# Performance work log

Hardware: AMD Instinct MI355X
Metric: run time of the kernel (lower is better)

The kernel has to match this reference:

```python
import jax, jax.numpy as jnp
import numpy as np

B, S, E, R = 128, 16, 512, 1000
_SCALE = np.float32(1.0 / np.sqrt(E))


def setup_inputs() -> dict:
    key = jax.random.key(0)
    ks = jax.random.split(key, 12)
    s = 1.0 / np.sqrt(E)
    u = lambda k, shape: jax.random.uniform(k, shape, jnp.float32, -s, s)
    emb = jax.random.normal(ks[0], (R + 1, E), jnp.float32).at[R].set(0.0)  # padding_idx row = 0
    return {
        "tokens": jax.random.randint(ks[11], (B, S), 0, R),
        "emb": emb,
        "W_ih": u(ks[1], (3 * E, E)), "W_hh": u(ks[2], (3 * E, E)),
        "b_ih": u(ks[3], (3 * E,)), "b_hh": u(ks[4], (3 * E,)),
        "w_fc": u(ks[5], (E,)), "b_fc": u(ks[6], ()),
        "Wq": u(ks[7], (E, E)), "bq": u(ks[8], (E,)),
        "Wk": u(ks[9], (E, E)), "bk": u(ks[10], (E,)),
    }


def _gru_step(x, h, W_ih, W_hh, b_ih, b_hh):
    # torch GRU cell: gates stacked as [r; z; n]
    gi = x @ W_ih.T + b_ih
    gh = h @ W_hh.T + b_hh
    ir, iz, inn = jnp.split(gi, 3, axis=-1)
    hr, hz, hn = jnp.split(gh, 3, axis=-1)
    r = jax.nn.sigmoid(ir + hr)
    z = jax.nn.sigmoid(iz + hz)
    n = jnp.tanh(inn + r * hn)
    return (1.0 - z) * n + z * h


def _attention(x, emb, Wq, bq, Wk, bk):
    # x: [B,1,E]; key = fc_k(cat(relation_emb, x)); scores = q k^T / sqrt(E)
    Bn = x.shape[0]
    rel = jnp.broadcast_to(emb[:R][None], (Bn, R, E))
    all_emb = jnp.concatenate([rel, x], axis=1)        # [B,R+1,E]
    q = x @ Wq.T + bq
    k = all_emb @ Wk.T + bk
    scores = jnp.einsum('bqe,bke->bqk', q, k) * _SCALE  # [B,1,R+1]
    return scores, all_emb


def _entropy(scores):
    lp = jax.nn.log_softmax(scores, axis=-1)
    return -jnp.sum(jnp.exp(lp) * lp, axis=-1)          # [B,1]


def _reduce(x, emb, W_ih, W_hh, b_ih, b_hh, w_fc, b_fc, Wq, bq, Wk, bk):
    Bn, L, Ed = x.shape
    if L > 2:
        # vectorized 2-step GRU over all adjacent pairs (replaces python while loop)
        h1 = _gru_step(x[:, :-1], jnp.zeros_like(x[:, :-1]), W_ih, W_hh, b_ih, b_hh)
        pairs = _gru_step(x[:, 1:], h1, W_ih, W_hh, b_ih, b_hh)   # [B,L-1,E]
        score = jax.nn.sigmoid(pairs @ w_fc + b_fc)               # [B,L-1]
        sel = jnp.argmax(score, axis=-1)                          # [B]
        barange = jnp.arange(Bn)
        pair = pairs[barange, sel][:, None]                       # [B,1,E]
        scores, all_emb = _attention(pair, emb, Wq, bq, Wk, bk)
        loss = _entropy(scores)
        prob = jax.nn.softmax(scores, axis=-1)                    # weightedAverage mask is all-False for seq_len=1
        merged = jnp.einsum('bqk,bke->bqe', prob, all_emb)[:, 0]  # [B,E]
        # output = inputs.detach().clone(); overwrite sel with merged; delete row sel+1
        out = jax.lax.stop_gradient(x).at[barange, sel].set(merged)
        j = jnp.arange(L - 1)[None]
        src = j + (j >= (sel + 1)[:, None])                       # skip zeroed row sel+1
        out = out[barange[:, None], src]                          # [B,L-1,E]
        return out, loss
    else:
        h1 = _gru_step(x[:, 0], jnp.zeros_like(x[:, 0]), W_ih, W_hh, b_ih, b_hh)
        h2 = _gru_step(x[:, 1], h1, W_ih, W_hh, b_ih, b_hh)
        return h2[:, None], jnp.zeros((Bn, 1), x.dtype)


def reference(tokens, emb, W_ih, W_hh, b_ih, b_hh, w_fc, b_fc, Wq, bq, Wk, bk):
    x = emb[tokens]                                               # [B,S,E]
    losses = []
    for _ in range(tokens.shape[1] - 1):
        x, l = _reduce(x, emb, W_ih, W_hh, b_ih, b_hh, w_fc, b_fc, Wq, bq, Wk, bk)
        losses.append(l)
    scores, _ = _attention(x, emb, Wq, bq, Wk, bk)                # x is [B,1,E]
    losses.append(_entropy(scores))
    return scores[:, 0], jnp.concatenate(losses, axis=-1)         # ([B,R+1], [B,S])
```

## Files before the change

### kernel.cpp

```cpp
#include <hip/hip_runtime.h>

#define B 128
#define S 16
#define E 512
#define R 1000
#define K3 1536
#define NW0 1920
#define NWS 256
#define NS (B * (R + 1))
#define SCALE 0.04419417382415922f

static __device__ __forceinline__ float sigm(float x) { return 1.f / (1.f + expf(-x)); }

static __device__ __forceinline__ float brsum(float v, float* sb) {
  int tid = threadIdx.x;
  sb[tid] = v; __syncthreads();
  for (int s = 128; s > 0; s >>= 1) {
    if (tid < s) sb[tid] += sb[tid + s];
    __syncthreads();
  }
  float r = sb[0]; __syncthreads();
  return r;
}
static __device__ __forceinline__ float brmax(float v, float* sb) {
  int tid = threadIdx.x;
  sb[tid] = v; __syncthreads();
  for (int s = 128; s > 0; s >>= 1) {
    if (tid < s) sb[tid] = fmaxf(sb[tid], sb[tid + s]);
    __syncthreads();
  }
  float r = sb[0]; __syncthreads();
  return r;
}
static __device__ __forceinline__ void brsum2(float v1, float v2, float* sb, float* sb2,
                                              float* o1, float* o2) {
  int tid = threadIdx.x;
  sb[tid] = v1; sb2[tid] = v2; __syncthreads();
  for (int s = 128; s > 0; s >>= 1) {
    if (tid < s) { sb[tid] += sb[tid + s]; sb2[tid] += sb2[tid + s]; }
    __syncthreads();
  }
  *o1 = sb[0]; *o2 = sb2[0]; __syncthreads();
}

#define TILE_FMA \
  _Pragma("unroll") \
  for (int k = 0; k < 16; ++k) { \
    float4 a4 = *(const float4*)&As[k][ty * 4]; \
    float4 w4 = *(const float4*)&Ws[k][tx * 4]; \
    acc[0][0] = fmaf(a4.x, w4.x, acc[0][0]); acc[0][1] = fmaf(a4.x, w4.y, acc[0][1]); \
    acc[0][2] = fmaf(a4.x, w4.z, acc[0][2]); acc[0][3] = fmaf(a4.x, w4.w, acc[0][3]); \
    acc[1][0] = fmaf(a4.y, w4.x, acc[1][0]); acc[1][1] = fmaf(a4.y, w4.y, acc[1][1]); \
    acc[1][2] = fmaf(a4.y, w4.z, acc[1][2]); acc[1][3] = fmaf(a4.y, w4.w, acc[1][3]); \
    acc[2][0] = fmaf(a4.z, w4.x, acc[2][0]); acc[2][1] = fmaf(a4.z, w4.y, acc[2][1]); \
    acc[2][2] = fmaf(a4.z, w4.z, acc[2][2]); acc[2][3] = fmaf(a4.z, w4.w, acc[2][3]); \
    acc[3][0] = fmaf(a4.w, w4.x, acc[3][0]); acc[3][1] = fmaf(a4.w, w4.y, acc[3][1]); \
    acc[3][2] = fmaf(a4.w, w4.z, acc[3][2]); acc[3][3] = fmaf(a4.w, w4.w, acc[3][3]); \
  }

#define TILE_FMA32 \
  _Pragma("unroll") \
  for (int k = 0; k < 16; ++k) { \
    float2 a2 = *(const float2*)&As[k][ty * 2]; \
    float4 w4 = *(const float4*)&Ws[k][tx * 4]; \
    acc[0][0] = fmaf(a2.x, w4.x, acc[0][0]); acc[0][1] = fmaf(a2.x, w4.y, acc[0][1]); \
    acc[0][2] = fmaf(a2.x, w4.z, acc[0][2]); acc[0][3] = fmaf(a2.x, w4.w, acc[0][3]); \
    acc[1][0] = fmaf(a2.y, w4.x, acc[1][0]); acc[1][1] = fmaf(a2.y, w4.y, acc[1][1]); \
    acc[1][2] = fmaf(a2.y, w4.z, acc[1][2]); acc[1][3] = fmaf(a2.y, w4.w, acc[1][3]); \
  }

__global__ __launch_bounds__(256) void k_gemm(const float* __restrict__ A, int lda, int M,
                                              const float* __restrict__ W, int N, int K,
                                              const float* __restrict__ bias, float scale,
                                              float* __restrict__ C, int ldc) {
  __shared__ float As[16][64];
  __shared__ float Ws[16][64];
  int tid = threadIdx.x;
  int mBase = blockIdx.y * 64;
  int nBase = blockIdx.x * 64;
  int tx = tid & 15, ty = tid >> 4;
  int li = tid & 63;
  int lk = (tid >> 6) * 4;
  float acc[4][4] = {{0.f,0.f,0.f,0.f},{0.f,0.f,0.f,0.f},{0.f,0.f,0.f,0.f},{0.f,0.f,0.f,0.f}};
  int m = mBase + li;
  const float* Arow = (m < M) ? (A + (size_t)m * lda) : nullptr;
  int n = nBase + li;
  const float* Wrow = (n < N) ? (W + (size_t)n * K) : nullptr;

  float4 av = Arow ? *(const float4*)(Arow + lk) : make_float4(0.f, 0.f, 0.f, 0.f);
  float4 wv = Wrow ? *(const float4*)(Wrow + lk) : make_float4(0.f, 0.f, 0.f, 0.f);

  for (int k0 = 0; k0 < K; k0 += 16) {
    As[lk + 0][li] = av.x; As[lk + 1][li] = av.y;
    As[lk + 2][li] = av.z; As[lk + 3][li] = av.w;
    Ws[lk + 0][li] = wv.x; Ws[lk + 1][li] = wv.y;
    Ws[lk + 2][li] = wv.z; Ws[lk + 3][li] = wv.w;
    __syncthreads();
    if (k0 + 16 < K) {
      av = Arow ? *(const float4*)(Arow + k0 + 16 + lk) : make_float4(0.f, 0.f, 0.f, 0.f);
      wv = Wrow ? *(const float4*)(Wrow + k0 + 16 + lk) : make_float4(0.f, 0.f, 0.f, 0.f);
    }
    TILE_FMA
    __syncthreads();
  }
#pragma unroll
  for (int r = 0; r < 4; ++r) {
    int mm = mBase + ty * 4 + r;
    if (mm >= M) continue;
#pragma unroll
    for (int c = 0; c < 4; ++c) {
      int nn = nBase + tx * 4 + c;
      if (nn >= N) continue;
      float v = acc[r][c] * scale;
      if (bias) v += bias[nn];
      C[(size_t)mm * ldc + nn] = v;
    }
  }
}

__global__ __launch_bounds__(256) void k_gemmD(const float* __restrict__ A, int lda, int M,
                                               const float* __restrict__ W1, int N1,
                                               const float* __restrict__ b1,
                                               float* __restrict__ C1, int ldc1,
                                               const float* __restrict__ W2, int N2,
                                               float* __restrict__ C2, int ldc2, int K) {
  __shared__ float As[16][64];
  __shared__ float Ws[16][64];
  int tid = threadIdx.x;
  int mBase = blockIdx.y * 64;
  int nBase = blockIdx.x * 64;
  int tx = tid & 15, ty = tid >> 4;
  int li = tid & 63;
  int lk = (tid >> 6) * 4;
  float acc[4][4] = {{0.f,0.f,0.f,0.f},{0.f,0.f,0.f,0.f},{0.f,0.f,0.f,0.f},{0.f,0.f,0.f,0.f}};
  int m = mBase + li;
  const float* Arow = (m < M) ? (A + (size_t)m * lda) : nullptr;
  int n = nBase + li;
  const float* Wrow = nullptr;
  if (n < N1) Wrow = W1 + (size_t)n * K;
  else if (n < N1 + N2) Wrow = W2 + (size_t)(n - N1) * K;

  float4 av = Arow ? *(const float4*)(Arow + lk) : make_float4(0.f, 0.f, 0.f, 0.f);
  float4 wv = Wrow ? *(const float4*)(Wrow + lk) : make_float4(0.f, 0.f, 0.f, 0.f);

  for (int k0 = 0; k0 < K; k0 += 16) {
    As[lk + 0][li] = av.x; As[lk + 1][li] = av.y;
    As[lk + 2][li] = av.z; As[lk + 3][li] = av.w;
    Ws[lk + 0][li] = wv.x; Ws[lk + 1][li] = wv.y;
    Ws[lk + 2][li] = wv.z; Ws[lk + 3][li] = wv.w;
    __syncthreads();
    if (k0 + 16 < K) {
      av = Arow ? *(const float4*)(Arow + k0 + 16 + lk) : make_float4(0.f, 0.f, 0.f, 0.f);
      wv = Wrow ? *(const float4*)(Wrow + k0 + 16 + lk) : make_float4(0.f, 0.f, 0.f, 0.f);
    }
    TILE_FMA
    __syncthreads();
  }
#pragma unroll
  for (int r = 0; r < 4; ++r) {
    int mm = mBase + ty * 4 + r;
    if (mm >= M) continue;
#pragma unroll
    for (int c = 0; c < 4; ++c) {
      int nn = nBase + tx * 4 + c;
      if (nn < N1) {
        float v = acc[r][c];
        if (b1) v += b1[nn];
        C1[(size_t)mm * ldc1 + nn] = v;
      } else if (nn < N1 + N2) {
        C2[(size_t)mm * ldc2 + (nn - N1)] = acc[r][c];
      }
    }
  }
}

static __device__ void dev_tr64(float (*t)[65], int tid, const float* __restrict__ src,
                                int Cc, float* __restrict__ dst, int ldd, int bx, int by) {
  int tx = tid & 15, ty = tid >> 4;
  int rb = by * 64, cb = bx * 64;
#pragma unroll
  for (int i = 0; i < 4; ++i) {
    int r = rb + ty + i * 16;
    float4 v = *(const float4*)(src + (size_t)r * Cc + cb + tx * 4);
    t[ty + i * 16][tx * 4 + 0] = v.x; t[ty + i * 16][tx * 4 + 1] = v.y;
    t[ty + i * 16][tx * 4 + 2] = v.z; t[ty + i * 16][tx * 4 + 3] = v.w;
  }
  __syncthreads();
#pragma unroll
  for (int i = 0; i < 4; ++i) {
    int c = cb + ty + i * 16;
    float4 v;
    v.x = t[tx * 4 + 0][ty + i * 16]; v.y = t[tx * 4 + 1][ty + i * 16];
    v.z = t[tx * 4 + 2][ty + i * 16]; v.w = t[tx * 4 + 3][ty + i * 16];
    *(float4*)(dst + (size_t)c * ldd + rb + tx * 4) = v;
  }
}

__global__ __launch_bounds__(256) void k_prep(const float* __restrict__ Wq,
                                              const float* __restrict__ Wk,
                                              const float* __restrict__ Wih,
                                              float* __restrict__ Wbig,
                                              int* __restrict__ pos,
                                              int* __restrict__ wlb,
                                              int* __restrict__ wlL,
                                              int* __restrict__ wlR,
                                              float* __restrict__ outp,
                                              float* __restrict__ Gbig,
                                              const float* __restrict__ bq,
                                              const float* __restrict__ bk,
                                              float* __restrict__ v12,
                                              float* __restrict__ bw,
                                              float* __restrict__ wv3,
                                              float* __restrict__ c0s) {
  __shared__ float t[64][65];
  int blk = blockIdx.x, tid = threadIdx.x;
  if (blk < 192) {
    dev_tr64(t, tid, Wih, E, Wbig + (size_t)1024 * K3, K3, blk & 7, blk >> 3);
  } else if (blk < 200) {
    int idx = (blk - 192) * 256 + tid;
    if (idx < B * 16) pos[idx] = idx & 15;
    if (idx < NW0) {
      wlb[idx] = idx / 15;
      int i = idx % 15;
      wlL[idx] = i;
      wlR[idx] = i + 1;
    }
    if (idx < B) outp[NS + idx * 16 + 14] = 0.f;
  } else if (blk < 208) {
    int idx = (blk - 200) * 256 + tid;
    for (int i = idx; i < 24 * K3; i += 8 * 256) Wbig[(size_t)1000 * K3 + i] = 0.f;
  } else if (blk < 272) {
    int j = blk - 208;
    int fT = (j & 7) * 64, iT = (j >> 3) * 64;
    float (*As)[64] = (float(*)[64])&t[0][0];
    float (*Ws)[64] = (float(*)[64])&t[20][0];
    int tx = tid & 15, ty = tid >> 4;
    int li = tid & 63, lk = (tid >> 6) * 4;
    float acc[4][4] = {{0.f,0.f,0.f,0.f},{0.f,0.f,0.f,0.f},{0.f,0.f,0.f,0.f},{0.f,0.f,0.f,0.f}};
    float a0 = Wq[(size_t)(lk + 0) * E + iT + li];
    float a1 = Wq[(size_t)(lk + 1) * E + iT + li];
    float a2 = Wq[(size_t)(lk + 2) * E + iT + li];
    float a3 = Wq[(size_t)(lk + 3) * E + iT + li];
    float w0 = Wk[(size_t)(lk + 0) * E + fT + li];
    float w1 = Wk[(size_t)(lk + 1) * E + fT + li];
    float w2 = Wk[(size_t)(lk + 2) * E + fT + li];
    float w3 = Wk[(size_t)(lk + 3) * E + fT + li];
    for (int e0 = 0; e0 < E; e0 += 16) {
      As[lk + 0][li] = a0; As[lk + 1][li] = a1;
      As[lk + 2][li] = a2; As[lk + 3][li] = a3;
      Ws[lk + 0][li] = w0; Ws[lk + 1][li] = w1;
      Ws[lk + 2][li] = w2; Ws[lk + 3][li] = w3;
      __syncthreads();
      if (e0 + 16 < E) {
        a0 = Wq[(size_t)(e0 + 16 + lk + 0) * E + iT + li];
        a1 = Wq[(size_t)(e0 + 16 + lk + 1) * E + iT + li];
        a2 = Wq[(size_t)(e0 + 16 + lk + 2) * E + iT + li];
        a3 = Wq[(size_t)(e0 + 16 + lk + 3) * E + iT + li];
        w0 = Wk[(size_t)(e0 + 16 + lk + 0) * E + fT + li];
        w1 = Wk[(size_t)(e0 + 16 + lk + 1) * E + fT + li];
        w2 = Wk[(size_t)(e0 + 16 + lk + 2) * E + fT + li];
        w3 = Wk[(size_t)(e0 + 16 + lk + 3) * E + fT + li];
      }
      TILE_FMA
      __syncthreads();
    }
#pragma unroll
    for (int r = 0; r < 4; ++r)
#pragma unroll
      for (int c = 0; c < 4; ++c)
        Gbig[(size_t)(1000 + iT + ty * 4 + r) * E + fT + tx * 4 + c] = acc[r][c];
  } else if (blk < 274) {
    int i = (blk - 272) * 256 + tid;
    float s = 0.f;
    for (int e = 0; e < E; ++e) s += Wq[(size_t)e * E + i] * bk[e] + bq[e] * Wk[(size_t)e * E + i];
    v12[i] = s;
  } else if (blk < 276) {
    int i = (blk - 274) * 256 + tid;
    float s = 0.f;
    for (int e = 0; e < E; ++e) s += bk[e] * Wq[(size_t)e * E + i];
    bw[i] = s;
  } else if (blk < 278) {
    int f = (blk - 276) * 256 + tid;
    float s = 0.f;
    for (int e = 0; e < E; ++e) s += bq[e] * Wk[(size_t)e * E + f];
    wv3[f] = s;
  } else {
    float* sb = &t[0][0];
    float p = 0.f;
    for (int e = tid; e < E; e += 256) p += bq[e] * bk[e];
    float s = brsum(p, sb);
    if (tid == 0) c0s[0] = s;
  }
}

__global__ __launch_bounds__(256) void k_setupB(const int* __restrict__ tokens,
                                                const float* __restrict__ Wbig,
                                                const float* __restrict__ bih,
                                                const float* __restrict__ bhh,
                                                const float* __restrict__ emb,
                                                const float* __restrict__ wv3,
                                                float* __restrict__ GI,
                                                float* __restrict__ H1V,
                                                float* __restrict__ SCT,
                                                float* __restrict__ gb) {
  int blk = blockIdx.x, tid = threadIdx.x;
  if (blk < 1000) {
    const float* ew = Wbig + (size_t)blk * K3;
    float* h = H1V + (size_t)blk * E;
    for (int e = tid; e < E; e += 256) {
      float g0 = ew[e] + bih[e];
      float g1 = ew[E + e] + bih[E + e];
      float g2 = ew[2 * E + e] + bih[2 * E + e];
      float r = sigm(g0 + bhh[e]);
      float z = sigm(g1 + bhh[E + e]);
      h[e] = (1.f - z) * tanhf(g2 + r * bhh[2 * E + e]);
    }
  } else if (blk < 1000 + B * S) {
    int p = blk - 1000;
    int tok = tokens[p];
    const float4* src = (const float4*)(Wbig + (size_t)tok * K3);
    const float4* bv = (const float4*)bih;
    float4* dst = (float4*)(GI + (size_t)p * K3);
    for (int i = tid; i < K3 / 4; i += 256) {
      float4 a = src[i], b = bv[i];
      dst[i] = make_float4(a.x + b.x, a.y + b.y, a.z + b.z, a.w + b.w);
    }
  } else if (blk < 1000 + B * S + 8) {
    int rb = blk - (1000 + B * S);
    for (int m = rb * 16; m < rb * 16 + 16; ++m) {
      float* r = SCT + (size_t)m * K3;
      for (int n = tid; n < 1512; n += 256) r[n] = 0.f;
    }
  } else {
    int r = (blk - (1000 + B * S + 8)) * 256 + tid;
    if (r < R) {
      const float* er = emb + (size_t)r * E;
      float s = 0.f;
      for (int f = 0; f < E; ++f) s += er[f] * wv3[f];
      gb[r] = s;
    }
  }
}

__global__ __launch_bounds__(256) void k_pairc0(const int* __restrict__ tokens,
                                                const float* __restrict__ GI,
                                                const float* __restrict__ GHCV,
                                                const float* __restrict__ H1V,
                                                const float* __restrict__ wfc,
                                                const float* __restrict__ bfc,
                                                float* __restrict__ PAIR,
                                                float* __restrict__ SCR,
                                                float* __restrict__ H1P,
                                                float* __restrict__ GHCP) {
  __shared__ float sb[256];
  int w = blockIdx.x, tid = threadIdx.x;
  int b = w / 15, i = w % 15;
  int lp = b * 16 + i;
  int tok = tokens[lp];
  const float* gr = GI + (size_t)(lp + 1) * K3;
  const float* gh = GHCV + (size_t)tok * K3;
  const float* h = H1V + (size_t)tok * E;
  float* ghp = GHCP + (size_t)lp * K3;
  float* hp = H1P + (size_t)lp * E;
  float* p = PAIR + (size_t)lp * E;
  float part = 0.f;
  for (int e = tid; e < E; e += 256) {
    float g0 = gh[e], g1 = gh[E + e], g2 = gh[2 * E + e], he = h[e];
    ghp[e] = g0; ghp[E + e] = g1; ghp[2 * E + e] = g2; hp[e] = he;
    float r = sigm(gr[e] + g0);
    float z = sigm(gr[E + e] + g1);
    float n = tanhf(gr[2 * E + e] + r * g2);
    float pv = (1.f - z) * n + z * he;
    p[e] = pv;
    part += pv * wfc[e];
  }
  float d = brsum(part, sb);
  if (tid == 0) SCR[lp] = sigm(d + bfc[0]);
}

__global__ __launch_bounds__(256) void k_h1c(const int* __restrict__ xdst,
                                             const float* __restrict__ GI,
                                             const float* __restrict__ bhh,
                                             float* __restrict__ H1P) {
  int p = xdst[blockIdx.x], tid = threadIdx.x;
  const float* gi = GI + (size_t)p * K3;
  float* h = H1P + (size_t)p * E;
  for (int e = tid; e < E; e += 256) {
    float r = sigm(gi[e] + bhh[e]);
    float z = sigm(gi[E + e] + bhh[E + e]);
    h[e] = (1.f - z) * tanhf(gi[2 * E + e] + r * bhh[2 * E + e]);
  }
}

__global__ __launch_bounds__(256) void k_ghcs(const int* __restrict__ xdst,
                                              const float* __restrict__ H1P,
                                              const float* __restrict__ Whh,
                                              float* __restrict__ GHCP) {
  __shared__ float As[16][32];
  __shared__ float Ws[16][64];
  __shared__ int sp[32];
  int tid = threadIdx.x;
  int nBase = blockIdx.x * 64;
  int mBase = blockIdx.y * 32;
  int kbeg = blockIdx.z * 256;
  if (tid < 32) sp[tid] = xdst[mBase + tid];
  __syncthreads();
  int tx = tid & 15, ty = tid >> 4;
  int ar = tid & 31, ak = (tid >> 5) * 2;
  int li = tid & 63, lk = (tid >> 6) * 4;
  float acc[2][4] = {{0.f,0.f,0.f,0.f},{0.f,0.f,0.f,0.f}};
  const float* Arow = H1P + (size_t)sp[ar] * E + kbeg;
  const float* Wrow = Whh + (size_t)(nBase + li) * E + kbeg;
  float2 av = *(const float2*)(Arow + ak);
  float4 wv = *(const float4*)(Wrow + lk);
  for (int k0 = 0; k0 < 256; k0 += 16) {
    As[ak + 0][ar] = av.x; As[ak + 1][ar] = av.y;
    Ws[lk + 0][li] = wv.x; Ws[lk + 1][li] = wv.y;
    Ws[lk + 2][li] = wv.z; Ws[lk + 3][li] = wv.w;
    __syncthreads();
    if (k0 + 16 < 256) {
      av = *(const float2*)(Arow + k0 + 16 + ak);
      wv = *(const float4*)(Wrow + k0 + 16 + lk);
    }
    TILE_FMA32
    __syncthreads();
  }
#pragma unroll
  for (int r = 0; r < 2; ++r) {
    size_t crow = (size_t)sp[ty * 2 + r] * K3;
#pragma unroll
    for (int c = 0; c < 4; ++c) {
      int nn = nBase + tx * 4 + c;
      atomicAdd(&GHCP[crow + nn], acc[r][c]);
    }
  }
}

__global__ __launch_bounds__(256) void k_pairc(const int* __restrict__ wlb,
                                               const int* __restrict__ wlL,
                                               const int* __restrict__ wlR,
                                               const float* __restrict__ GI,
                                               const float* __restrict__ GHCP,
                                               const float* __restrict__ H1P,
                                               const float* __restrict__ wfc,
                                               const float* __restrict__ bfc,
                                               float* __restrict__ PAIR,
                                               float* __restrict__ SCR) {
  __shared__ float sb[256];
  int w = blockIdx.x, tid = threadIdx.x;
  int b = wlb[w], ls = wlL[w], rs = wlR[w];
  int lp = b * 16 + ls;
  const float* gr = GI + (size_t)(b * 16 + rs) * K3;
  const float* gh = GHCP + (size_t)lp * K3;
  const float* h = H1P + (size_t)lp * E;
  float* p = PAIR + (size_t)lp * E;
  float part = 0.f;
  for (int e = tid; e < E; e += 256) {
    float r = sigm(gr[e] + gh[e]);
    float z = sigm(gr[E + e] + gh[E + e]);
    float n = tanhf(gr[2 * E + e] + r * gh[2 * E + e]);
    float pv = (1.f - z) * n + z * h[e];
    p[e] = pv;
    part += pv * wfc[e];
  }
  float d = brsum(part, sb);
  if (tid == 0) SCR[b * 16 + ls] = sigm(d + bfc[0]);
}

__global__ __launch_bounds__(256) void k_qscsel(const float* __restrict__ PAIR,
                                                const float* __restrict__ SCR,
                                                const int* __restrict__ pin,
                                                int* __restrict__ pout,
                                                int* __restrict__ wlb,
                                                int* __restrict__ wlL,
                                                int* __restrict__ wlR,
                                                int* __restrict__ xdst,
                                                const float* __restrict__ Gbig,
                                                float* __restrict__ SCT,
                                                float* __restrict__ GI,
                                                const float* __restrict__ bih,
                                                float* __restrict__ GHCP,
                                                const float* __restrict__ bhh,
                                                int P, int finalMode) {
  __shared__ float As[16][32];
  __shared__ float Ws[16][64];
  __shared__ int sxd[32];
  int tid = threadIdx.x;
  int nBase = blockIdx.x * 64;
  int mBase = blockIdx.y * 32;
  int kbeg = blockIdx.z * 256;
  if (tid < 32) {
    int b = mBase + tid;
    if (finalMode) {
      int xr = b * 16 + pin[b * 16];
      sxd[tid] = xr;
      if (blockIdx.x == 0 && blockIdx.z == 0) xdst[b] = xr;
    } else {
      int L = P + 1;
      int lp[16];
      for (int i = 0; i < L; ++i) lp[i] = pin[b * 16 + i];
      float best = -1e30f; int sel = 0;
      for (int i = 0; i < P; ++i) {
        float v = SCR[b * 16 + lp[i]];
        if (v > best) { best = v; sel = i; }
      }
      int r1i = (sel + 2 < L) ? sel + 2 : L - 1;
      int l1 = lp[sel], r1 = lp[r1i];
      int l0 = (sel > 0) ? lp[sel - 1] : l1;
      int r0 = (sel > 0) ? lp[sel] : r1;
      sxd[tid] = b * 16 + l1;
      if (blockIdx.x == 0 && blockIdx.z == 0) {
        wlb[2 * b] = b;     wlL[2 * b] = l0;     wlR[2 * b] = r0;
        wlb[2 * b + 1] = b; wlL[2 * b + 1] = l1; wlR[2 * b + 1] = r1;
        xdst[b] = b * 16 + l1;
        for (int i = 0; i < L - 1; ++i)
          pout[b * 16 + i] = (i <= sel) ? lp[i] : lp[i + 1];
      }
    }
  }
  __syncthreads();
  if (!finalMode && blockIdx.z == 1) {
    if (blockIdx.x < 16) {
#pragma unroll
      for (int r = 0; r < 2; ++r) {
        float* g = GI + (size_t)sxd[blockIdx.x * 2 + r] * K3;
        for (int i = tid; i < K3; i += 256) g[i] = bih[i];
      }
    } else {
#pragma unroll
      for (int r = 0; r < 4; ++r) {
        float* g = GHCP + (size_t)sxd[(blockIdx.x - 16) * 4 + r] * K3;
        for (int i = tid; i < K3; i += 256) g[i] = bhh[i];
      }
    }
  }
  int tx = tid & 15, ty = tid >> 4;
  int ar = tid & 31, ak = (tid >> 5) * 2;
  int li = tid & 63, lk = (tid >> 6) * 4;
  float acc[2][4] = {{0.f,0.f,0.f,0.f},{0.f,0.f,0.f,0.f}};
  const float* Arow = PAIR + (size_t)sxd[ar] * E + kbeg;
  int n = nBase + li;
  const float* Wrow = (n < 1512) ? (Gbig + (size_t)n * E + kbeg) : nullptr;
  float2 av = *(const float2*)(Arow + ak);
  float4 wv = Wrow ? *(const float4*)(Wrow + lk) : make_float4(0.f, 0.f, 0.f, 0.f);
  for (int k0 = 0; k0 < 256; k0 += 16) {
    As[ak + 0][ar] = av.x; As[ak + 1][ar] = av.y;
    Ws[lk + 0][li] = wv.x; Ws[lk + 1][li] = wv.y;
    Ws[lk + 2][li] = wv.z; Ws[lk + 3][li] = wv.w;
    __syncthreads();
    if (k0 + 16 < 256) {
      av = *(const float2*)(Arow + k0 + 16 + ak);
      wv = Wrow ? *(const float4*)(Wrow + k0 + 16 + lk) : make_float4(0.f, 0.f, 0.f, 0.f);
    }
    TILE_FMA32
    __syncthreads();
  }
#pragma unroll
  for (int r = 0; r < 2; ++r) {
    int mm = mBase + ty * 2 + r;
#pragma unroll
    for (int c = 0; c < 4; ++c) {
      int nn = nBase + tx * 4 + c;
      if (nn < 1512) atomicAdd(&SCT[(size_t)mm * K3 + nn], acc[r][c]);
    }
  }
}

__global__ __launch_bounds__(256) void k_sm(float* __restrict__ SCT,
                                            const float* __restrict__ PAIR,
                                            const int* __restrict__ xdst,
                                            const float* __restrict__ v12,
                                            const float* __restrict__ bw,
                                            const float* __restrict__ c0s,
                                            float* __restrict__ outp,
                                            float* __restrict__ A2,
                                            const float* __restrict__ gb,
                                            int t, int finalMode) {
  __shared__ float sb[256];
  __shared__ float sb2[256];
  __shared__ float sps[E];
  int b = blockIdx.x, tid = threadIdx.x;
  float* row = SCT + (size_t)b * K3;
  int xr = xdst[b];
  const float* sp = PAIR + (size_t)xr * E;
  for (int i = tid; i < E; i += 256) sps[i] = sp[i];
  __syncthreads();
  float part = 0.f, pbw = 0.f;
  for (int i = tid; i < E; i += 256) {
    part += sps[i] * (row[1000 + i] + v12[i]);
    pbw += sps[i] * bw[i];
  }
  float ps, pb;
  brsum2(part, pbw, sb, sb2, &ps, &pb);
  float last = (ps + c0s[0]) * SCALE;
  float shift = pb + c0s[0];
  float s[4];
  float ml = last;
#pragma unroll
  for (int q = 0; q < 4; ++q) {
    int j = tid + q * 256;
    s[q] = (j < 1000) ? (row[j] + gb[j] + shift) * SCALE : -1e30f;
    ml = fmaxf(ml, s[q]);
  }
  float mx = brmax(ml, sb);
  float zp = 0.f, s1p = 0.f;
#pragma unroll
  for (int q = 0; q < 4; ++q) {
    int j = tid + q * 256;
    if (j < 1000) { float e = expf(s[q] - mx); zp += e; s1p += e * s[q]; }
  }
  if (tid == 0) { float e = expf(last - mx); zp += e; s1p += e * last; }
  float z, s1;
  brsum2(zp, s1p, sb, sb2, &z, &s1);
  if (tid == 0) outp[NS + b * 16 + t] = mx + logf(z) - s1 / z;
  if (!finalMode) {
    float inv = 1.f / z;
    float* a = A2 + (size_t)b * K3;
#pragma unroll
    for (int q = 0; q < 4; ++q) {
      int j = tid + q * 256;
      if (j < 1000) a[j] = expf(s[q] - mx) * inv;
    }
    if (tid < 24) a[1000 + tid] = 0.f;
    float pr = expf(last - mx) * inv;
    for (int i = tid; i < E; i += 256) a[1024 + i] = pr * sps[i];
    for (int n2 = tid; n2 < 1512; n2 += 256) row[n2] = 0.f;
  } else {
    float* so = outp + (size_t)b * (R + 1);
#pragma unroll
    for (int q = 0; q < 4; ++q) {
      int j = tid + q * 256;
      if (j < 1000) so[j] = s[q];
    }
    if (tid == 0) so[R] = last;
  }
}

__global__ __launch_bounds__(256) void k_giup(const float* __restrict__ A2,
                                              const float* __restrict__ Wbig,
                                              float* __restrict__ GI,
                                              const int* __restrict__ xdst) {
  __shared__ float As[16][32];
  __shared__ float Ws[16][64];
  int tid = threadIdx.x;
  int nBase = blockIdx.x * 64;
  int mBase = blockIdx.y * 32;
  int kbeg = blockIdx.z * 384;
  int kend = kbeg + 384;
  int tx = tid & 15, ty = tid >> 4;
  int ar = tid & 31, ak = (tid >> 5) * 2;
  int li = tid & 63, wr = tid >> 6;
  float acc[2][4] = {{0.f,0.f,0.f,0.f},{0.f,0.f,0.f,0.f}};
  const float* Arow = A2 + (size_t)(mBase + ar) * K3;
  float2 av = *(const float2*)(Arow + kbeg + ak);
  float w0 = Wbig[(size_t)(kbeg + wr * 4 + 0) * K3 + nBase + li];
  float w1 = Wbig[(size_t)(kbeg + wr * 4 + 1) * K3 + nBase + li];
  float w2 = Wbig[(size_t)(kbeg + wr * 4 + 2) * K3 + nBase + li];
  float w3 = Wbig[(size_t)(kbeg + wr * 4 + 3) * K3 + nBase + li];
  for (int k0 = kbeg; k0 < kend; k0 += 16) {
    As[ak + 0][ar] = av.x; As[ak + 1][ar] = av.y;
    Ws[wr * 4 + 0][li] = w0; Ws[wr * 4 + 1][li] = w1;
    Ws[wr * 4 + 2][li] = w2; Ws[wr * 4 + 3][li] = w3;
    __syncthreads();
    if (k0 + 16 < kend) {
      av = *(const float2*)(Arow + k0 + 16 + ak);
      w0 = Wbig[(size_t)(k0 + 16 + wr * 4 + 0) * K3 + nBase + li];
      w1 = Wbig[(size_t)(k0 + 16 + wr * 4 + 1) * K3 + nBase + li];
      w2 = Wbig[(size_t)(k0 + 16 + wr * 4 + 2) * K3 + nBase + li];
      w3 = Wbig[(size_t)(k0 + 16 + wr * 4 + 3) * K3 + nBase + li];
    }
    TILE_FMA32
    __syncthreads();
  }
#pragma unroll
  for (int r = 0; r < 2; ++r) {
    int mm = mBase + ty * 2 + r;
    size_t crow = (size_t)xdst[mm] * K3;
#pragma unroll
    for (int c = 0; c < 4; ++c) {
      int nn = nBase + tx * 4 + c;
      atomicAdd(&GI[crow + nn], acc[r][c]);
    }
  }
}

extern "C" void kernel_launch(void* const* d_in, const int* in_sizes, int n_in,
                              void* d_out, int out_size, void* d_ws, size_t ws_size,
                              hipStream_t stream) {
  (void)in_sizes; (void)n_in; (void)out_size; (void)ws_size;
  const int* tokens = (const int*)d_in[0];
  const float* emb = (const float*)d_in[1];
  const float* W_ih = (const float*)d_in[2];
  const float* W_hh = (const float*)d_in[3];
  const float* b_ih = (const float*)d_in[4];
  const float* b_hh = (const float*)d_in[5];
  const float* w_fc = (const float*)d_in[6];
  const float* b_fc = (const float*)d_in[7];
  const float* Wq = (const float*)d_in[8];
  const float* bq = (const float*)d_in[9];
  const float* Wk = (const float*)d_in[10];
  const float* bk = (const float*)d_in[11];
  float* out = (float*)d_out;

  float* ws = (float*)d_ws;
  size_t o = 0;
  float* GI = ws + o;    o += (size_t)B * S * K3;
  float* GHCP = ws + o;  o += (size_t)B * S * K3;
  float* H1P = ws + o;   o += (size_t)B * S * E;
  float* PAIR = ws + o;  o += (size_t)B * S * E;
  float* Wbig = ws + o;  o += (size_t)K3 * K3;
  float* Gbig = ws + o;  o += (size_t)1512 * E;
  float* H1V = ws + o;   o += (size_t)1024 * E;
  float* GHCV = ws + o;  o += (size_t)1024 * K3;
  float* SCT = ws + o;   o += (size_t)B * K3;
  float* A2 = ws + o;    o += (size_t)B * K3;
  float* gb = ws + o;    o += 1024;
  float* v12 = ws + o;   o += 512;
  float* bw = ws + o;    o += 512;
  float* wv3 = ws + o;   o += 512;
  float* c0s = ws + o;   o += 16;
  float* SCR = ws + o;   o += B * 16;
  int* pos0 = (int*)(ws + o); o += B * 16;
  int* pos1 = (int*)(ws + o); o += B * 16;
  int* wlb = (int*)(ws + o);  o += NW0;
  int* wlL = (int*)(ws + o);  o += NW0;
  int* wlR = (int*)(ws + o);  o += NW0;
  int* xdst = (int*)(ws + o); o += B;

  k_prep<<<279, 256, 0, stream>>>(Wq, Wk, W_ih, Wbig, pos0, wlb, wlL, wlR, out,
                                  Gbig, bq, bk, v12, bw, wv3, c0s);
  k_gemmD<<<dim3(32, 16), 256, 0, stream>>>(emb, E, R, W_ih, K3, nullptr, Wbig, K3,
                                            Gbig + (size_t)1000 * E, 512, Gbig, E, E);
  k_setupB<<<1000 + B * S + 8 + 4, 256, 0, stream>>>(tokens, Wbig, b_ih, b_hh, emb,
                                                     wv3, GI, H1V, SCT, gb);
  k_gemm<<<dim3(24, 16), 256, 0, stream>>>(H1V, E, 1000, W_hh, K3, E, b_hh, 1.f,
                                           GHCV, K3);
  k_pairc0<<<NW0, 256, 0, stream>>>(tokens, GI, GHCV, H1V, w_fc, b_fc, PAIR, SCR,
                                    H1P, GHCP);

  for (int t = 0; t < 14; ++t) {
    int* pin = (t & 1) ? pos1 : pos0;
    int* pout = (t & 1) ? pos0 : pos1;
    k_qscsel<<<dim3(24, 4, 2), 256, 0, stream>>>(PAIR, SCR, pin, pout, wlb, wlL, wlR,
                                                 xdst, Gbig, SCT, GI, b_ih, GHCP, b_hh,
                                                 15 - t, 0);
    k_sm<<<B, 256, 0, stream>>>(SCT, PAIR, xdst, v12, bw, c0s, out, A2, gb, t, 0);
    k_giup<<<dim3(24, 4, 4), 256, 0, stream>>>(A2, Wbig, GI, xdst);
    k_h1c<<<B, 256, 0, stream>>>(xdst, GI, b_hh, H1P);
    k_ghcs<<<dim3(24, 4, 2), 256, 0, stream>>>(xdst, H1P, W_hh, GHCP);
    k_pairc<<<NWS, 256, 0, stream>>>(wlb, wlL, wlR, GI, GHCP, H1P, w_fc, b_fc, PAIR, SCR);
  }

  k_qscsel<<<dim3(24, 4, 2), 256, 0, stream>>>(PAIR, SCR, pos0, pos1, wlb, wlL, wlR,
                                               xdst, Gbig, SCT, GI, b_ih, GHCP, b_hh,
                                               1, 1);
  k_sm<<<B, 256, 0, stream>>>(SCT, PAIR, xdst, v12, bw, c0s, out, A2, gb, 15, 1);
}
```

Measured before the change: 1.326 ms.

## Fuse GRU h1 computation into k_giup via last-block counters and vectorize bias init

Removes the separate k_h1c launch per step. Each k_giup block bumps a per-tile atomic counter, and the last of the 12 contributing blocks computes the h1 GRU cell for that 32x64 slice from the accumulated GI values. The counters are reset in k_sm. The bias-initialisation writes in k_qscsel now use float4 stores and are spread over more blocks. This saves launch overhead and a pass over memory, but depends on correct acquire/release ordering of the atomics.

Result: slower. 1.394 ms (+5.1%).

```diff
diff --git a/kernel.cpp b/kernel.cpp
--- a/kernel.cpp
+++ b/kernel.cpp
@@ -376,20 +376,6 @@
   }
   float d = brsum(part, sb);
   if (tid == 0) SCR[lp] = sigm(d + bfc[0]);
-}
-
-__global__ __launch_bounds__(256) void k_h1c(const int* __restrict__ xdst,
-                                             const float* __restrict__ GI,
-                                             const float* __restrict__ bhh,
-                                             float* __restrict__ H1P) {
-  int p = xdst[blockIdx.x], tid = threadIdx.x;
-  const float* gi = GI + (size_t)p * K3;
-  float* h = H1P + (size_t)p * E;
-  for (int e = tid; e < E; e += 256) {
-    float r = sigm(gi[e] + bhh[e]);
-    float z = sigm(gi[E + e] + bhh[E + e]);
-    h[e] = (1.f - z) * tanhf(gi[2 * E + e] + r * bhh[2 * E + e]);
-  }
 }
 
 __global__ __launch_bounds__(256) void k_ghcs(const int* __restrict__ xdst,
@@ -519,18 +505,20 @@
     }
   }
   __syncthreads();
-  if (!finalMode && blockIdx.z == 1) {
-    if (blockIdx.x < 16) {
+  if (!finalMode) {
+    if (blockIdx.z == 1 && blockIdx.x < 16) {
 #pragma unroll
       for (int r = 0; r < 2; ++r) {
-        float* g = GI + (size_t)sxd[blockIdx.x * 2 + r] * K3;
-        for (int i = tid; i < K3; i += 256) g[i] = bih[i];
+        float4* g = (float4*)(GI + (size_t)sxd[blockIdx.x * 2 + r] * K3);
+        const float4* s = (const float4*)bih;
+        for (int i = tid; i < K3 / 4; i += 256) g[i] = s[i];
       }
-    } else {
-#pragma unroll
-      for (int r = 0; r < 4; ++r) {
-        float* g = GHCP + (size_t)sxd[(blockIdx.x - 16) * 4 + r] * K3;
-        for (int i = tid; i < K3; i += 256) g[i] = bhh[i];
+    } else if (blockIdx.z == 0 && blockIdx.x >= 8) {
+#pragma unroll
+      for (int r = 0; r < 2; ++r) {
+        float4* g = (float4*)(GHCP + (size_t)sxd[(blockIdx.x - 8) * 2 + r] * K3);
+        const float4* s = (const float4*)bhh;
+        for (int i = tid; i < K3 / 4; i += 256) g[i] = s[i];
       }
     }
   }
@@ -575,11 +563,13 @@
                                             float* __restrict__ outp,
                                             float* __restrict__ A2,
                                             const float* __restrict__ gb,
+                                            int* __restrict__ cnt,
                                             int t, int finalMode) {
   __shared__ float sb[256];
   __shared__ float sb2[256];
   __shared__ float sps[E];
   int b = blockIdx.x, tid = threadIdx.x;
+  if (!finalMode && b == 0 && tid < 32) cnt[tid] = 0;
   float* row = SCT + (size_t)b * K3;
   int xr = xdst[b];
   const float* sp = PAIR + (size_t)xr * E;
@@ -639,9 +629,13 @@
 __global__ __launch_bounds__(256) void k_giup(const float* __restrict__ A2,
                                               const float* __restrict__ Wbig,
                                               float* __restrict__ GI,
-                                              const int* __restrict__ xdst) {
+                                              const int* __restrict__ xdst,
+                                              const float* __restrict__ bhh,
+                                              float* __restrict__ H1P,
+                                              int* __restrict__ cnt) {
   __shared__ float As[16][32];
   __shared__ float Ws[16][64];
+  __shared__ int lastFlag;
   int tid = threadIdx.x;
   int nBase = blockIdx.x * 64;
   int mBase = blockIdx.y * 32;
@@ -680,6 +674,28 @@
     for (int c = 0; c < 4; ++c) {
       int nn = nBase + tx * 4 + c;
       atomicAdd(&GI[crow + nn], acc[r][c]);
+    }
+  }
+  __syncthreads();
+  int g = blockIdx.x & 7;
+  int ci = blockIdx.y * 8 + g;
+  if (tid == 0) {
+    int old = __hip_atomic_fetch_add(&cnt[ci], 1, __ATOMIC_ACQ_REL, __HIP_MEMORY_SCOPE_AGENT);
+    lastFlag = (old == 11) ? 1 : 0;
+  }
+  __syncthreads();
+  if (lastFlag) {
+    int yB = blockIdx.y * 32;
+    for (int i = tid; i < 32 * 64; i += 256) {
+      int b = yB + (i >> 6);
+      int e = g * 64 + (i & 63);
+      const float* gi = GI + (size_t)xdst[b] * K3;
+      float v0 = __hip_atomic_load(&gi[e], __ATOMIC_RELAXED, __HIP_MEMORY_SCOPE_AGENT);
+      float v1 = __hip_atomic_load(&gi[E + e], __ATOMIC_RELAXED, __HIP_MEMORY_SCOPE_AGENT);
+      float v2 = __hip_atomic_load(&gi[2 * E + e], __ATOMIC_RELAXED, __HIP_MEMORY_SCOPE_AGENT);
+      float r = sigm(v0 + bhh[e]);
+      float z = sigm(v1 + bhh[E + e]);
+      H1P[(size_t)xdst[b] * E + e] = (1.f - z) * tanhf(v2 + r * bhh[2 * E + e]);
     }
   }
 }
@@ -726,6 +742,7 @@
   int* wlL = (int*)(ws + o);  o += NW0;
   int* wlR = (int*)(ws + o);  o += NW0;
   int* xdst = (int*)(ws + o); o += B;
+  int* cnt = (int*)(ws + o);  o += 32;
 
   k_prep<<<279, 256, 0, stream>>>(Wq, Wk, W_ih, Wbig, pos0, wlb, wlL, wlR, out,
                                   Gbig, bq, bk, v12, bw, wv3, c0s);
@@ -744,9 +761,8 @@
     k_qscsel<<<dim3(24, 4, 2), 256, 0, stream>>>(PAIR, SCR, pin, pout, wlb, wlL, wlR,
                                                  xdst, Gbig, SCT, GI, b_ih, GHCP, b_hh,
                                                  15 - t, 0);
-    k_sm<<<B, 256, 0, stream>>>(SCT, PAIR, xdst, v12, bw, c0s, out, A2, gb, t, 0);
-    k_giup<<<dim3(24, 4, 4), 256, 0, stream>>>(A2, Wbig, GI, xdst);
-    k_h1c<<<B, 256, 0, stream>>>(xdst, GI, b_hh, H1P);
+    k_sm<<<B, 256, 0, stream>>>(SCT, PAIR, xdst, v12, bw, c0s, out, A2, gb, cnt, t, 0);
+    k_giup<<<dim3(24, 4, 4), 256, 0, stream>>>(A2, Wbig, GI, xdst, b_hh, H1P, cnt);
     k_ghcs<<<dim3(24, 4, 2), 256, 0, stream>>>(xdst, H1P, W_hh, GHCP);
     k_pairc<<<NWS, 256, 0, stream>>>(wlb, wlL, wlR, GI, GHCP, H1P, w_fc, b_fc, PAIR, SCR);
   }
@@ -754,5 +770,5 @@
   k_qscsel<<<dim3(24, 4, 2), 256, 0, stream>>>(PAIR, SCR, pos0, pos1, wlb, wlL, wlR,
                                                xdst, Gbig, SCT, GI, b_ih, GHCP, b_hh,
                                                1, 1);
-  k_sm<<<B, 256, 0, stream>>>(SCT, PAIR, xdst, v12, bw, c0s, out, A2, gb, 15, 1);
-}
+  k_sm<<<B, 256, 0, stream>>>(SCT, PAIR, xdst, v12, bw, c0s, out, A2, gb, cnt, 15, 1);
+}
```
